# Kernel optimization log

Measured on AMD Instinct MI355X. Metric: run time of the kernel, lower is better.

The kernel has to match this reference:

```python
import jax, jax.numpy as jnp
import numpy as np

HALF_PI = np.float32(np.pi / 2.0)
EPS = 1e-8

def feature_map(x):
    # [B, L] -> [B, L, 2]: standard quantum-inspired embedding
    return jnp.stack([jnp.cos(HALF_PI * x), jnp.sin(HALF_PI * x)], axis=-1)

def setup_inputs() -> dict:
    key = jax.random.key(0)
    k1, k2, k3, k4 = jax.random.split(key, 4)
    B, L, F, D, C = 32768, 256, 2, 32, 10
    x = jax.random.uniform(k1, (B, L), dtype=jnp.float32)
    core0 = jax.random.normal(k2, (F, 1, D), dtype=jnp.float32) * 0.1
    cores_mid = jax.random.normal(k3, (L - 2, F, D, D), dtype=jnp.float32) * 0.1
    coreN = jax.random.normal(k4, (F, D, C), dtype=jnp.float32) * 0.1
    return {"x": x, "core0": core0, "cores_mid": cores_mid, "coreN": coreN}

def reference(x, core0, cores_mid, coreN):
    feats = feature_map(x)                      # [B, L, F]
    # first site: M = v0 @ A0  -> [B, D]
    M0 = jnp.einsum('bf,fd->bd', feats[:, 0, :], core0[:, 0, :])

    # sequential scan over middle sites with per-step L2 normalization
    vs = jnp.transpose(feats[:, 1:-1, :], (1, 0, 2))  # [L-2, B, F]

    def step(M, inputs):
        v, A = inputs                           # v: [B,F], A: [F,D,D]
        M = jnp.einsum('ba,bf,fac->bc', M, v, A)
        M = M / (jnp.linalg.norm(M, axis=1, keepdims=True) + EPS)
        return M, None

    M, _ = jax.lax.scan(step, M0, (vs, cores_mid))

    # last site and readout
    final = jnp.einsum('bf,fac->bac', feats[:, -1, :], coreN)  # [B, D, C]
    logits = jnp.einsum('ba,bac->bc', M, final)                # [B, C]
    return logits
```

## Files before the change

kernel.cpp:

```cpp
#include <hip/hip_runtime.h>
#include <hip/hip_bf16.h>

#define B_TOTAL   32768
#define L_SITES   256
#define N_MID     254
#define HALF_PI_F 1.57079632679489662f
#define EPS_NORM  1e-8f

#define WS_FRAG 0
#define WS_C0   520192
#define WS_CN   520256

typedef short bf16x8 __attribute__((ext_vector_type(8)));
typedef float f32x4  __attribute__((ext_vector_type(4)));

__device__ __host__ __forceinline__ int pi_perm(int quad, int j) {
    return (j < 4) ? (quad * 4 + j) : (16 + quad * 4 + (j - 4));
}

__device__ __forceinline__ unsigned short f2bf(float f) {
    unsigned u = __builtin_bit_cast(unsigned, f);
    u += 0x7FFFu + ((u >> 16) & 1u);
    return (unsigned short)(u >> 16);
}
__device__ __forceinline__ float bf2f(unsigned short h) {
    unsigned u = ((unsigned)h) << 16;
    return __builtin_bit_cast(float, u);
}
__device__ __forceinline__ bf16x8 asbf(uint4 u) {
    return __builtin_bit_cast(bf16x8, u);
}
__device__ __forceinline__ void psincos(float x, float* s, float* c) {
    float u = x * x;
    float sp = fmaf(u, -3.5988432352121e-6f, 1.6044118478736e-4f);
    sp = fmaf(u, sp, -4.6817541353187e-3f);
    sp = fmaf(u, sp, 7.9692626246167e-2f);
    sp = fmaf(u, sp, -6.4596409750625e-1f);
    sp = fmaf(u, sp, 1.5707963267949f);
    *s = x * sp;
    float cp = fmaf(u, 4.7108749076366e-7f, -2.5202042373061e-5f);
    cp = fmaf(u, cp, 9.1926027483943e-4f);
    cp = fmaf(u, cp, -2.0863480763353e-2f);
    cp = fmaf(u, cp, 2.5366950790105e-1f);
    cp = fmaf(u, cp, -1.2337005501362f);
    *c = fmaf(u, cp, 1.0f);
}
__device__ __forceinline__ unsigned pkbf2(float a, float b) {
    float2 p; p.x = a; p.y = b;
    __hip_bfloat162 h2 = __float22bfloat162_rn(p);
    unsigned u;
    __builtin_memcpy(&u, &h2, 4);
    return u;
}
__device__ __forceinline__ void split8(const float* v, bf16x8& hi, bf16x8& lo) {
    uint4 H, L;
    unsigned* hp = (unsigned*)&H;
    unsigned* lp = (unsigned*)&L;
    #pragma unroll
    for (int d = 0; d < 4; ++d) {
        float a = v[2 * d], b = v[2 * d + 1];
        unsigned hb = pkbf2(a, b);
        float h0 = __builtin_bit_cast(float, hb << 16);
        float h1 = __builtin_bit_cast(float, hb & 0xFFFF0000u);
        hp[d] = hb;
        lp[d] = pkbf2(a - h0, b - h1);
    }
    hi = __builtin_bit_cast(bf16x8, H);
    lo = __builtin_bit_cast(bf16x8, L);
}
__device__ __forceinline__ bool detect_bf16(const unsigned* x_raw, int lane) {
    unsigned v = x_raw[lane];
    return __ballot((v & 0xFFFFu) >= 0x4000u) == 0ull;
}

__global__ __launch_bounds__(256)
void aux_all(const void* __restrict__ x_in, const void* __restrict__ c0_in,
             const void* __restrict__ am_in, const void* __restrict__ cn_in,
             float* __restrict__ ws) {
    const int lane = threadIdx.x & 63;
    const bool bf = detect_bf16((const unsigned*)x_in, lane);
    const int b = blockIdx.x;

    if (b < 2 * N_MID) {
        const int t  = b >> 1;
        const int kh = b & 1;
        __shared__ float amS[32][33];
        if (!bf) {
            const float* src = (const float*)am_in + (size_t)t * 2048 + kh * 1024;
            for (int idx = threadIdx.x; idx < 1024; idx += 256)
                amS[idx >> 5][idx & 31] = src[idx];
        } else {
            const unsigned short* src =
                (const unsigned short*)am_in + (size_t)t * 2048 + kh * 1024;
            for (int idx = threadIdx.x; idx < 1024; idx += 256)
                amS[idx >> 5][idx & 31] = bf2f(src[idx]);
        }
        __syncthreads();
        const int l  = threadIdx.x & 63;
        const int qi = threadIdx.x >> 6;
        const int h  = qi >> 1;
        const int p  = qi & 1;
        const int q  = h * 4 + kh * 2 + p;
        const int m  = h * 16 + (l & 15);
        const int kb = (l >> 4) * 8;
        unsigned dw[4];
        #pragma unroll
        for (int d = 0; d < 4; ++d) {
            unsigned e01[2];
            #pragma unroll
            for (int s = 0; s < 2; ++s) {
                int k = kb + 2 * d + s;
                int a = pi_perm(k >> 3, k & 7);
                float v = amS[a][m];
                unsigned short hi = f2bf(v);
                e01[s] = (p == 0) ? hi : f2bf(v - bf2f(hi));
            }
            dw[d] = e01[0] | (e01[1] << 16);
        }
        uint4 o; o.x = dw[0]; o.y = dw[1]; o.z = dw[2]; o.w = dw[3];
        ((uint4*)ws)[(size_t)(t * 8 + q) * 64 + l] = o;
    } else {
        for (int i = threadIdx.x; i < 640; i += 256) {
            if (i < 64)
                ws[WS_C0 + i] = bf ? bf2f(((const unsigned short*)c0_in)[i])
                                   : ((const float*)c0_in)[i];
            ws[WS_CN + i] = bf ? bf2f(((const unsigned short*)cn_in)[i])
                               : ((const float*)cn_in)[i];
        }
    }
}

__global__ __launch_bounds__(256, 2)
void mps_mfma(const float* __restrict__ ws, const void* __restrict__ x_in,
              void* __restrict__ out) {
    __shared__ float xs[L_SITES][64];
    const int lane = threadIdx.x & 63;
    const int w    = threadIdx.x >> 6;
    const int r    = lane & 15;
    const int quad = lane >> 4;
    const int bb   = blockIdx.x * 64;
    const int bl   = w * 16 + r;
    const int b0   = bb + w * 16;
    const uint4* __restrict__ BF = (const uint4*)ws;
    const bool bf = detect_bf16((const unsigned*)x_in, lane);

    if (!bf) {
        const float4* x4 = (const float4*)x_in;
        const int row = threadIdx.x >> 2;
        const int q   = threadIdx.x & 3;
        #pragma unroll
        for (int u = 0; u < 16; ++u) {
            int c4 = q + u * 4;
            float4 v = x4[(size_t)(bb + row) * (L_SITES / 4) + c4];
            xs[c4 * 4 + 0][row] = v.x;
            xs[c4 * 4 + 1][row] = v.y;
            xs[c4 * 4 + 2][row] = v.z;
            xs[c4 * 4 + 3][row] = v.w;
        }
    } else {
        const uint4* x8 = (const uint4*)x_in;
        const int row = threadIdx.x >> 2;
        const int q   = threadIdx.x & 3;
        #pragma unroll
        for (int u = 0; u < 8; ++u) {
            int c8 = q + u * 4;
            uint4 v = x8[(size_t)(bb + row) * (L_SITES / 8) + c8];
            const unsigned short* e = (const unsigned short*)&v;
            #pragma unroll
            for (int k = 0; k < 8; ++k) xs[c8 * 8 + k][row] = bf2f(e[k]);
        }
    }
    __syncthreads();

    float mm[8];
    {
        float x0 = xs[0][bl];
        float sn, cs; psincos(x0, &sn, &cs);
        const float* c0 = ws + WS_C0;
        #pragma unroll
        for (int j = 0; j < 8; ++j) {
            int a = pi_perm(quad, j);
            mm[j] = cs * c0[a] + sn * c0[32 + a];
        }
    }
    float ct, st;
    psincos(xs[1][bl], &st, &ct);
    float xn = xs[2][bl];

    #pragma unroll 1
    for (int t = 0; t < N_MID; ++t) {
        const uint4* F = BF + (size_t)t * 512 + lane;
        uint4 f0 = F[0];    uint4 f1 = F[64];
        uint4 f2 = F[128];  uint4 f3 = F[192];
        uint4 f4 = F[256];  uint4 f5 = F[320];
        uint4 f6 = F[384];  uint4 f7 = F[448];

        float ctn, stn; psincos(xn, &stn, &ctn);
        int xr = t + 3; if (xr > 255) xr = 255;
        float xn2 = xs[xr][bl];

        bf16x8 mh, ml;
        split8(mm, mh, ml);
        const f32x4 z = {0.f, 0.f, 0.f, 0.f};
        __builtin_amdgcn_s_setprio(1);
        f32x4 p00 = __builtin_amdgcn_mfma_f32_16x16x32_bf16(asbf(f0), mh, z, 0, 0, 0);
        f32x4 p01 = __builtin_amdgcn_mfma_f32_16x16x32_bf16(asbf(f2), mh, z, 0, 0, 0);
        f32x4 p10 = __builtin_amdgcn_mfma_f32_16x16x32_bf16(asbf(f4), mh, z, 0, 0, 0);
        f32x4 p11 = __builtin_amdgcn_mfma_f32_16x16x32_bf16(asbf(f6), mh, z, 0, 0, 0);
        p00 = __builtin_amdgcn_mfma_f32_16x16x32_bf16(asbf(f1), mh, p00, 0, 0, 0);
        p01 = __builtin_amdgcn_mfma_f32_16x16x32_bf16(asbf(f3), mh, p01, 0, 0, 0);
        p10 = __builtin_amdgcn_mfma_f32_16x16x32_bf16(asbf(f5), mh, p10, 0, 0, 0);
        p11 = __builtin_amdgcn_mfma_f32_16x16x32_bf16(asbf(f7), mh, p11, 0, 0, 0);
        p00 = __builtin_amdgcn_mfma_f32_16x16x32_bf16(asbf(f0), ml, p00, 0, 0, 0);
        p01 = __builtin_amdgcn_mfma_f32_16x16x32_bf16(asbf(f2), ml, p01, 0, 0, 0);
        p10 = __builtin_amdgcn_mfma_f32_16x16x32_bf16(asbf(f4), ml, p10, 0, 0, 0);
        p11 = __builtin_amdgcn_mfma_f32_16x16x32_bf16(asbf(f6), ml, p11, 0, 0, 0);
        __builtin_amdgcn_s_setprio(0);
        #pragma unroll
        for (int j = 0; j < 4; ++j) {
            mm[j]     = fmaf(st, p01[j], ct * p00[j]);
            mm[4 + j] = fmaf(st, p11[j], ct * p10[j]);
        }

        if (((t & 7) == 7) || (t == N_MID - 1)) {
            float ss = 0.f;
            #pragma unroll
            for (int j = 0; j < 8; ++j) ss = fmaf(mm[j], mm[j], ss);
            ss += __shfl_xor(ss, 16);
            ss += __shfl_xor(ss, 32);
            float kk = 1.0f / (sqrtf(ss) + EPS_NORM);
            #pragma unroll
            for (int j = 0; j < 8; ++j) mm[j] *= kk;
        }

        ct = ctn; st = stn; xn = xn2;
    }

    {
        float xN = xs[L_SITES - 1][bl];
        float sN, cN; psincos(xN, &sN, &cN);
        const float* kn = ws + WS_CN;
        float acc[10];
        #pragma unroll
        for (int c = 0; c < 10; ++c) acc[c] = 0.f;
        #pragma unroll
        for (int j = 0; j < 8; ++j) {
            int a = pi_perm(quad, j);
            float Ma = mm[j];
            #pragma unroll
            for (int c = 0; c < 10; ++c) {
                float fin = cN * kn[a * 10 + c] + sN * kn[320 + a * 10 + c];
                acc[c] = fmaf(Ma, fin, acc[c]);
            }
        }
        #pragma unroll
        for (int c = 0; c < 10; ++c) {
            acc[c] += __shfl_xor(acc[c], 16);
            acc[c] += __shfl_xor(acc[c], 32);
        }
        if (quad == 0) {
            if (bf) {
                __hip_bfloat16* o = (__hip_bfloat16*)out;
                #pragma unroll
                for (int c = 0; c < 10; ++c)
                    o[(size_t)(b0 + r) * 10 + c] = __float2bfloat16(acc[c]);
            } else {
                float* o = (float*)out;
                #pragma unroll
                for (int c = 0; c < 10; ++c)
                    o[(size_t)(b0 + r) * 10 + c] = acc[c];
            }
        }
    }
}

extern "C" void kernel_launch(void* const* d_in, const int* in_sizes, int n_in,
                              void* d_out, int out_size, void* d_ws, size_t ws_size,
                              hipStream_t stream) {
    float* ws = (float*)d_ws;
    aux_all<<<2 * N_MID + 1, 256, 0, stream>>>(d_in[0], d_in[1], d_in[2], d_in[3], ws);
    mps_mfma<<<512, 256, 0, stream>>>(ws, d_in[0], d_out);
}
```

Before: 219.8 us.

## Double-buffer per-step core fragment loads across unrolled scan iterations

```diff
diff --git a/kernel.cpp b/kernel.cpp
--- a/kernel.cpp
+++ b/kernel.cpp
@@ -130,7 +130,8 @@
     }
 }
 
-__global__ __launch_bounds__(256, 2)
+__global__ __launch_bounds__(256)
+__attribute__((amdgpu_waves_per_eu(2, 2)))
 void mps_mfma(const float* __restrict__ ws, const void* __restrict__ x_in,
               void* __restrict__ out) {
     __shared__ float xs[L_SITES][64];
@@ -172,6 +173,49 @@
     }
     __syncthreads();
 
+#define LOADB(A0, A1, A2, A3, A4, A5, A6, A7, STEP)                                \
+    {                                                                              \
+        const uint4* F_ = BF + (size_t)(STEP) * 512 + lane;                        \
+        A0 = F_[0];    A1 = F_[64];   A2 = F_[128];  A3 = F_[192];                 \
+        A4 = F_[256];  A5 = F_[320];  A6 = F_[384];  A7 = F_[448];                 \
+    }
+
+#define DO_STEP(CT, ST, Q0, Q1, Q2, Q3, Q4, Q5, Q6, Q7, DONORM)                    \
+    {                                                                              \
+        bf16x8 mh, ml;                                                             \
+        split8(mm, mh, ml);                                                        \
+        const f32x4 z = {0.f, 0.f, 0.f, 0.f};                                      \
+        __builtin_amdgcn_s_setprio(1);                                             \
+        f32x4 p00 = __builtin_amdgcn_mfma_f32_16x16x32_bf16(asbf(Q0), mh, z, 0, 0, 0);    \
+        f32x4 p01 = __builtin_amdgcn_mfma_f32_16x16x32_bf16(asbf(Q2), mh, z, 0, 0, 0);    \
+        f32x4 p10 = __builtin_amdgcn_mfma_f32_16x16x32_bf16(asbf(Q4), mh, z, 0, 0, 0);    \
+        f32x4 p11 = __builtin_amdgcn_mfma_f32_16x16x32_bf16(asbf(Q6), mh, z, 0, 0, 0);    \
+        p00 = __builtin_amdgcn_mfma_f32_16x16x32_bf16(asbf(Q1), mh, p00, 0, 0, 0); \
+        p01 = __builtin_amdgcn_mfma_f32_16x16x32_bf16(asbf(Q3), mh, p01, 0, 0, 0); \
+        p10 = __builtin_amdgcn_mfma_f32_16x16x32_bf16(asbf(Q5), mh, p10, 0, 0, 0); \
+        p11 = __builtin_amdgcn_mfma_f32_16x16x32_bf16(asbf(Q7), mh, p11, 0, 0, 0); \
+        p00 = __builtin_amdgcn_mfma_f32_16x16x32_bf16(asbf(Q0), ml, p00, 0, 0, 0); \
+        p01 = __builtin_amdgcn_mfma_f32_16x16x32_bf16(asbf(Q2), ml, p01, 0, 0, 0); \
+        p10 = __builtin_amdgcn_mfma_f32_16x16x32_bf16(asbf(Q4), ml, p10, 0, 0, 0); \
+        p11 = __builtin_amdgcn_mfma_f32_16x16x32_bf16(asbf(Q6), ml, p11, 0, 0, 0); \
+        __builtin_amdgcn_s_setprio(0);                                             \
+        _Pragma("unroll")                                                          \
+        for (int j = 0; j < 4; ++j) {                                              \
+            mm[j]     = fmaf((ST), p01[j], (CT) * p00[j]);                         \
+            mm[4 + j] = fmaf((ST), p11[j], (CT) * p10[j]);                         \
+        }                                                                          \
+        if (DONORM) {                                                              \
+            float ss = 0.f;                                                        \
+            _Pragma("unroll")                                                      \
+            for (int j = 0; j < 8; ++j) ss = fmaf(mm[j], mm[j], ss);               \
+            ss += __shfl_xor(ss, 16);                                              \
+            ss += __shfl_xor(ss, 32);                                              \
+            float kk = 1.0f / (sqrtf(ss) + EPS_NORM);                              \
+            _Pragma("unroll")                                                      \
+            for (int j = 0; j < 8; ++j) mm[j] *= kk;                               \
+        }                                                                          \
+    }
+
     float mm[8];
     {
         float x0 = xs[0][bl];
@@ -183,58 +227,30 @@
             mm[j] = cs * c0[a] + sn * c0[32 + a];
         }
     }
-    float ct, st;
-    psincos(xs[1][bl], &st, &ct);
-    float xn = xs[2][bl];
+    float ct0, st0;
+    psincos(xs[1][bl], &st0, &ct0);
+    float x1 = xs[2][bl];
+
+    uint4 fa0, fa1, fa2, fa3, fa4, fa5, fa6, fa7;
+    uint4 fb0, fb1, fb2, fb3, fb4, fb5, fb6, fb7;
+    LOADB(fa0, fa1, fa2, fa3, fa4, fa5, fa6, fa7, 0)
 
     #pragma unroll 1
-    for (int t = 0; t < N_MID; ++t) {
-        const uint4* F = BF + (size_t)t * 512 + lane;
-        uint4 f0 = F[0];    uint4 f1 = F[64];
-        uint4 f2 = F[128];  uint4 f3 = F[192];
-        uint4 f4 = F[256];  uint4 f5 = F[320];
-        uint4 f6 = F[384];  uint4 f7 = F[448];
-
-        float ctn, stn; psincos(xn, &stn, &ctn);
-        int xr = t + 3; if (xr > 255) xr = 255;
-        float xn2 = xs[xr][bl];
-
-        bf16x8 mh, ml;
-        split8(mm, mh, ml);
-        const f32x4 z = {0.f, 0.f, 0.f, 0.f};
-        __builtin_amdgcn_s_setprio(1);
-        f32x4 p00 = __builtin_amdgcn_mfma_f32_16x16x32_bf16(asbf(f0), mh, z, 0, 0, 0);
-        f32x4 p01 = __builtin_amdgcn_mfma_f32_16x16x32_bf16(asbf(f2), mh, z, 0, 0, 0);
-        f32x4 p10 = __builtin_amdgcn_mfma_f32_16x16x32_bf16(asbf(f4), mh, z, 0, 0, 0);
-        f32x4 p11 = __builtin_amdgcn_mfma_f32_16x16x32_bf16(asbf(f6), mh, z, 0, 0, 0);
-        p00 = __builtin_amdgcn_mfma_f32_16x16x32_bf16(asbf(f1), mh, p00, 0, 0, 0);
-        p01 = __builtin_amdgcn_mfma_f32_16x16x32_bf16(asbf(f3), mh, p01, 0, 0, 0);
-        p10 = __builtin_amdgcn_mfma_f32_16x16x32_bf16(asbf(f5), mh, p10, 0, 0, 0);
-        p11 = __builtin_amdgcn_mfma_f32_16x16x32_bf16(asbf(f7), mh, p11, 0, 0, 0);
-        p00 = __builtin_amdgcn_mfma_f32_16x16x32_bf16(asbf(f0), ml, p00, 0, 0, 0);
-        p01 = __builtin_amdgcn_mfma_f32_16x16x32_bf16(asbf(f2), ml, p01, 0, 0, 0);
-        p10 = __builtin_amdgcn_mfma_f32_16x16x32_bf16(asbf(f4), ml, p10, 0, 0, 0);
-        p11 = __builtin_amdgcn_mfma_f32_16x16x32_bf16(asbf(f6), ml, p11, 0, 0, 0);
-        __builtin_amdgcn_s_setprio(0);
-        #pragma unroll
-        for (int j = 0; j < 4; ++j) {
-            mm[j]     = fmaf(st, p01[j], ct * p00[j]);
-            mm[4 + j] = fmaf(st, p11[j], ct * p10[j]);
-        }
-
-        if (((t & 7) == 7) || (t == N_MID - 1)) {
-            float ss = 0.f;
-            #pragma unroll
-            for (int j = 0; j < 8; ++j) ss = fmaf(mm[j], mm[j], ss);
-            ss += __shfl_xor(ss, 16);
-            ss += __shfl_xor(ss, 32);
-            float kk = 1.0f / (sqrtf(ss) + EPS_NORM);
-            #pragma unroll
-            for (int j = 0; j < 8; ++j) mm[j] *= kk;
-        }
-
-        ct = ctn; st = stn; xn = xn2;
-    }
+    for (int t = 0; t < N_MID; t += 2) {
+        LOADB(fb0, fb1, fb2, fb3, fb4, fb5, fb6, fb7, t + 1)
+        float x2 = xs[t + 3][bl];
+        float ct1, st1; psincos(x1, &st1, &ct1);
+        DO_STEP(ct0, st0, fa0, fa1, fa2, fa3, fa4, fa5, fa6, fa7, false)
+
+        LOADB(fa0, fa1, fa2, fa3, fa4, fa5, fa6, fa7, t + 2)
+        int xr = t + 4; if (xr > 255) xr = 255;
+        x1 = xs[xr][bl];
+        psincos(x2, &st0, &ct0);
+        DO_STEP(ct1, st1, fb0, fb1, fb2, fb3, fb4, fb5, fb6, fb7,
+                (((t + 1) & 7) == 7) || (t + 1 == N_MID - 1))
+    }
+#undef DO_STEP
+#undef LOADB
 
     {
         float xN = xs[L_SITES - 1][bl];
```

New measurement: 216.3 us. No clear change (-1.6%).

## Precompute pairwise products of adjacent MPS cores to halve sequential steps

Applied to the files above, without the earlier changes.

```diff
diff --git a/kernel.cpp b/kernel.cpp
--- a/kernel.cpp
+++ b/kernel.cpp
@@ -4,6 +4,7 @@
 #define B_TOTAL   32768
 #define L_SITES   256
 #define N_MID     254
+#define N_PAIR    127
 #define HALF_PI_F 1.57079632679489662f
 #define EPS_NORM  1e-8f
 
@@ -81,44 +82,63 @@
     const bool bf = detect_bf16((const unsigned*)x_in, lane);
     const int b = blockIdx.x;
 
-    if (b < 2 * N_MID) {
-        const int t  = b >> 1;
-        const int kh = b & 1;
-        __shared__ float amS[32][33];
-        if (!bf) {
-            const float* src = (const float*)am_in + (size_t)t * 2048 + kh * 1024;
-            for (int idx = threadIdx.x; idx < 1024; idx += 256)
-                amS[idx >> 5][idx & 31] = src[idx];
-        } else {
-            const unsigned short* src =
-                (const unsigned short*)am_in + (size_t)t * 2048 + kh * 1024;
-            for (int idx = threadIdx.x; idx < 1024; idx += 256)
-                amS[idx >> 5][idx & 31] = bf2f(src[idx]);
+    if (b < N_PAIR) {
+        const int p = b;
+        __shared__ float a1t[2][32][32];
+        __shared__ float a2 [2][32][32];
+        const unsigned short* us = (const unsigned short*)am_in;
+        const float* fl = (const float*)am_in;
+        for (int idx = threadIdx.x; idx < 4096; idx += 256) {
+            int which = idx >> 11;
+            int off   = idx & 2047;
+            size_t gi = (size_t)(2 * p + which) * 2048 + off;
+            float v = bf ? bf2f(us[gi]) : fl[gi];
+            if (which == 0) {
+                int f = off >> 10, a = (off >> 5) & 31, e = off & 31;
+                a1t[f][e][a] = v;
+            } else {
+                ((float*)a2)[off] = v;
+            }
         }
         __syncthreads();
-        const int l  = threadIdx.x & 63;
-        const int qi = threadIdx.x >> 6;
-        const int h  = qi >> 1;
-        const int p  = qi & 1;
-        const int q  = h * 4 + kh * 2 + p;
-        const int m  = h * 16 + (l & 15);
-        const int kb = (l >> 4) * 8;
-        unsigned dw[4];
+        const int l   = threadIdx.x & 63;
+        const int c2b = threadIdx.x >> 6;
+        const int f1  = c2b >> 1, f2 = c2b & 1;
+        const int m0  = l & 15;
+        const int m1  = 16 + (l & 15);
+        unsigned H0[4], L0[4], H1[4], L1[4];
         #pragma unroll
         for (int d = 0; d < 4; ++d) {
-            unsigned e01[2];
+            unsigned h0 = 0, l0 = 0, h1 = 0, l1 = 0;
             #pragma unroll
             for (int s = 0; s < 2; ++s) {
-                int k = kb + 2 * d + s;
+                int k = (l >> 4) * 8 + 2 * d + s;
                 int a = pi_perm(k >> 3, k & 7);
-                float v = amS[a][m];
-                unsigned short hi = f2bf(v);
-                e01[s] = (p == 0) ? hi : f2bf(v - bf2f(hi));
+                float v0 = 0.f, v1 = 0.f;
+                #pragma unroll 8
+                for (int e = 0; e < 32; ++e) {
+                    float t = a1t[f1][e][a];
+                    v0 = fmaf(t, a2[f2][e][m0], v0);
+                    v1 = fmaf(t, a2[f2][e][m1], v1);
+                }
+                unsigned short vh0 = f2bf(v0);
+                unsigned short vl0 = f2bf(v0 - bf2f(vh0));
+                unsigned short vh1 = f2bf(v1);
+                unsigned short vl1 = f2bf(v1 - bf2f(vh1));
+                h0 |= ((unsigned)vh0) << (16 * s);
+                l0 |= ((unsigned)vl0) << (16 * s);
+                h1 |= ((unsigned)vh1) << (16 * s);
+                l1 |= ((unsigned)vl1) << (16 * s);
             }
-            dw[d] = e01[0] | (e01[1] << 16);
-        }
-        uint4 o; o.x = dw[0]; o.y = dw[1]; o.z = dw[2]; o.w = dw[3];
-        ((uint4*)ws)[(size_t)(t * 8 + q) * 64 + l] = o;
+            H0[d] = h0; L0[d] = l0; H1[d] = h1; L1[d] = l1;
+        }
+        uint4* o = (uint4*)ws;
+        const size_t base = ((size_t)p * 16 + c2b * 4) * 64 + l;
+        uint4 u;
+        u.x = H0[0]; u.y = H0[1]; u.z = H0[2]; u.w = H0[3]; o[base]       = u;
+        u.x = L0[0]; u.y = L0[1]; u.z = L0[2]; u.w = L0[3]; o[base + 64]  = u;
+        u.x = H1[0]; u.y = H1[1]; u.z = H1[2]; u.w = H1[3]; o[base + 128] = u;
+        u.x = L1[0]; u.y = L1[1]; u.z = L1[2]; u.w = L1[3]; o[base + 192] = u;
     } else {
         for (int i = threadIdx.x; i < 640; i += 256) {
             if (i < 64)
@@ -130,10 +150,11 @@
     }
 }
 
-__global__ __launch_bounds__(256, 2)
+__global__ __launch_bounds__(256)
+__attribute__((amdgpu_waves_per_eu(2, 2)))
 void mps_mfma(const float* __restrict__ ws, const void* __restrict__ x_in,
               void* __restrict__ out) {
-    __shared__ float xs[L_SITES][64];
+    __shared__ float xs[L_SITES][65];
     const int lane = threadIdx.x & 63;
     const int w    = threadIdx.x >> 6;
     const int r    = lane & 15;
@@ -183,46 +204,59 @@
             mm[j] = cs * c0[a] + sn * c0[32 + a];
         }
     }
-    float ct, st;
-    psincos(xs[1][bl], &st, &ct);
-    float xn = xs[2][bl];
 
     #pragma unroll 1
-    for (int t = 0; t < N_MID; ++t) {
-        const uint4* F = BF + (size_t)t * 512 + lane;
-        uint4 f0 = F[0];    uint4 f1 = F[64];
-        uint4 f2 = F[128];  uint4 f3 = F[192];
-        uint4 f4 = F[256];  uint4 f5 = F[320];
-        uint4 f6 = F[384];  uint4 f7 = F[448];
-
-        float ctn, stn; psincos(xn, &stn, &ctn);
-        int xr = t + 3; if (xr > 255) xr = 255;
-        float xn2 = xs[xr][bl];
+    for (int p = 0; p < N_PAIR; ++p) {
+        const uint4* F = BF + (size_t)p * 1024 + lane;
+        uint4 g0  = F[0];    uint4 g1  = F[64];   uint4 g2  = F[128];  uint4 g3  = F[192];
+        uint4 g4  = F[256];  uint4 g5  = F[320];  uint4 g6  = F[384];  uint4 g7  = F[448];
+        uint4 g8  = F[512];  uint4 g9  = F[576];  uint4 g10 = F[640];  uint4 g11 = F[704];
+        uint4 g12 = F[768];  uint4 g13 = F[832];  uint4 g14 = F[896];  uint4 g15 = F[960];
+
+        float s1, c1, s2, c2;
+        psincos(xs[2 * p + 1][bl], &s1, &c1);
+        psincos(xs[2 * p + 2][bl], &s2, &c2);
 
         bf16x8 mh, ml;
         split8(mm, mh, ml);
         const f32x4 z = {0.f, 0.f, 0.f, 0.f};
         __builtin_amdgcn_s_setprio(1);
-        f32x4 p00 = __builtin_amdgcn_mfma_f32_16x16x32_bf16(asbf(f0), mh, z, 0, 0, 0);
-        f32x4 p01 = __builtin_amdgcn_mfma_f32_16x16x32_bf16(asbf(f2), mh, z, 0, 0, 0);
-        f32x4 p10 = __builtin_amdgcn_mfma_f32_16x16x32_bf16(asbf(f4), mh, z, 0, 0, 0);
-        f32x4 p11 = __builtin_amdgcn_mfma_f32_16x16x32_bf16(asbf(f6), mh, z, 0, 0, 0);
-        p00 = __builtin_amdgcn_mfma_f32_16x16x32_bf16(asbf(f1), mh, p00, 0, 0, 0);
-        p01 = __builtin_amdgcn_mfma_f32_16x16x32_bf16(asbf(f3), mh, p01, 0, 0, 0);
-        p10 = __builtin_amdgcn_mfma_f32_16x16x32_bf16(asbf(f5), mh, p10, 0, 0, 0);
-        p11 = __builtin_amdgcn_mfma_f32_16x16x32_bf16(asbf(f7), mh, p11, 0, 0, 0);
-        p00 = __builtin_amdgcn_mfma_f32_16x16x32_bf16(asbf(f0), ml, p00, 0, 0, 0);
-        p01 = __builtin_amdgcn_mfma_f32_16x16x32_bf16(asbf(f2), ml, p01, 0, 0, 0);
-        p10 = __builtin_amdgcn_mfma_f32_16x16x32_bf16(asbf(f4), ml, p10, 0, 0, 0);
-        p11 = __builtin_amdgcn_mfma_f32_16x16x32_bf16(asbf(f6), ml, p11, 0, 0, 0);
+        f32x4 A00 = __builtin_amdgcn_mfma_f32_16x16x32_bf16(asbf(g0),  mh, z, 0, 0, 0);
+        f32x4 A01 = __builtin_amdgcn_mfma_f32_16x16x32_bf16(asbf(g2),  mh, z, 0, 0, 0);
+        f32x4 A10 = __builtin_amdgcn_mfma_f32_16x16x32_bf16(asbf(g4),  mh, z, 0, 0, 0);
+        f32x4 A11 = __builtin_amdgcn_mfma_f32_16x16x32_bf16(asbf(g6),  mh, z, 0, 0, 0);
+        f32x4 A20 = __builtin_amdgcn_mfma_f32_16x16x32_bf16(asbf(g8),  mh, z, 0, 0, 0);
+        f32x4 A21 = __builtin_amdgcn_mfma_f32_16x16x32_bf16(asbf(g10), mh, z, 0, 0, 0);
+        f32x4 A30 = __builtin_amdgcn_mfma_f32_16x16x32_bf16(asbf(g12), mh, z, 0, 0, 0);
+        f32x4 A31 = __builtin_amdgcn_mfma_f32_16x16x32_bf16(asbf(g14), mh, z, 0, 0, 0);
+        A00 = __builtin_amdgcn_mfma_f32_16x16x32_bf16(asbf(g1),  mh, A00, 0, 0, 0);
+        A01 = __builtin_amdgcn_mfma_f32_16x16x32_bf16(asbf(g3),  mh, A01, 0, 0, 0);
+        A10 = __builtin_amdgcn_mfma_f32_16x16x32_bf16(asbf(g5),  mh, A10, 0, 0, 0);
+        A11 = __builtin_amdgcn_mfma_f32_16x16x32_bf16(asbf(g7),  mh, A11, 0, 0, 0);
+        A20 = __builtin_amdgcn_mfma_f32_16x16x32_bf16(asbf(g9),  mh, A20, 0, 0, 0);
+        A21 = __builtin_amdgcn_mfma_f32_16x16x32_bf16(asbf(g11), mh, A21, 0, 0, 0);
+        A30 = __builtin_amdgcn_mfma_f32_16x16x32_bf16(asbf(g13), mh, A30, 0, 0, 0);
+        A31 = __builtin_amdgcn_mfma_f32_16x16x32_bf16(asbf(g15), mh, A31, 0, 0, 0);
+        A00 = __builtin_amdgcn_mfma_f32_16x16x32_bf16(asbf(g0),  ml, A00, 0, 0, 0);
+        A01 = __builtin_amdgcn_mfma_f32_16x16x32_bf16(asbf(g2),  ml, A01, 0, 0, 0);
+        A10 = __builtin_amdgcn_mfma_f32_16x16x32_bf16(asbf(g4),  ml, A10, 0, 0, 0);
+        A11 = __builtin_amdgcn_mfma_f32_16x16x32_bf16(asbf(g6),  ml, A11, 0, 0, 0);
+        A20 = __builtin_amdgcn_mfma_f32_16x16x32_bf16(asbf(g8),  ml, A20, 0, 0, 0);
+        A21 = __builtin_amdgcn_mfma_f32_16x16x32_bf16(asbf(g10), ml, A21, 0, 0, 0);
+        A30 = __builtin_amdgcn_mfma_f32_16x16x32_bf16(asbf(g12), ml, A30, 0, 0, 0);
+        A31 = __builtin_amdgcn_mfma_f32_16x16x32_bf16(asbf(g14), ml, A31, 0, 0, 0);
         __builtin_amdgcn_s_setprio(0);
+
+        float wcc = c1 * c2, wcs = c1 * s2, wsc = s1 * c2, wss = s1 * s2;
         #pragma unroll
         for (int j = 0; j < 4; ++j) {
-            mm[j]     = fmaf(st, p01[j], ct * p00[j]);
-            mm[4 + j] = fmaf(st, p11[j], ct * p10[j]);
-        }
-
-        if (((t & 7) == 7) || (t == N_MID - 1)) {
+            mm[j]     = fmaf(wss, A30[j], fmaf(wsc, A20[j],
+                        fmaf(wcs, A10[j], wcc * A00[j])));
+            mm[4 + j] = fmaf(wss, A31[j], fmaf(wsc, A21[j],
+                        fmaf(wcs, A11[j], wcc * A01[j])));
+        }
+
+        if (((p & 3) == 3) || (p == N_PAIR - 1)) {
             float ss = 0.f;
             #pragma unroll
             for (int j = 0; j < 8; ++j) ss = fmaf(mm[j], mm[j], ss);
@@ -232,8 +266,6 @@
             #pragma unroll
             for (int j = 0; j < 8; ++j) mm[j] *= kk;
         }
-
-        ct = ctn; st = stn; xn = xn2;
     }
 
     {
@@ -278,6 +310,6 @@
                               void* d_out, int out_size, void* d_ws, size_t ws_size,
                               hipStream_t stream) {
     float* ws = (float*)d_ws;
-    aux_all<<<2 * N_MID + 1, 256, 0, stream>>>(d_in[0], d_in[1], d_in[2], d_in[3], ws);
+    aux_all<<<N_PAIR + 1, 256, 0, stream>>>(d_in[0], d_in[1], d_in[2], d_in[3], ws);
     mps_mfma<<<512, 256, 0, stream>>>(ws, d_in[0], d_out);
 }
```

After: 223.6 us. No clear change (+1.7%).
